# Kernel optimization log

Measured on AMD Instinct MI355X. Metric: run time of the kernel, lower is better.

## Reference

```python
import jax, jax.numpy as jnp
import numpy as np

B, EMBED, HEADS, T = 2, 512, 8, 2048
DH = EMBED // HEADS
EPS = 1e-5
# NOTE: torch code computes embed_dim // num_heads ** 0.5 == 512 // sqrt(8)
SCALE = EMBED // HEADS ** 0.5  # = 181.0, reproduced faithfully


def ws_conv1x1(x, w, b, mask):
    # weight-standardized 1x1 conv; w: [O, I], x: [B, I, T], mask: [B, T]
    mu = jnp.mean(w, axis=1, keepdims=True)
    var = jnp.var(w, axis=1, keepdims=True)
    wn = (w - mu) * jax.lax.rsqrt(var + EPS)
    x = x * mask[:, None, :].astype(x.dtype)
    return jnp.einsum('oi,bit->bot', wn, x) + b[None, :, None]


def ln_head(x, g, b):
    # per-head LayerNorm over head dim; x: [B, H, DH, T], normalized over DH
    xt = jnp.swapaxes(x, -1, -2)  # [B, H, T, DH]
    mu = jnp.mean(xt, axis=-1, keepdims=True)
    var = jnp.var(xt, axis=-1, keepdims=True)
    xn = (xt - mu) * jax.lax.rsqrt(var + EPS) * g + b
    return jnp.swapaxes(xn, -1, -2)


def setup_inputs():
    key = jax.random.key(0)
    ks = jax.random.split(key, 12)
    sc = 1.0 / np.sqrt(EMBED)
    d = {
        'q': jax.random.normal(ks[0], (B, EMBED, T), jnp.float32),
        'k': jax.random.normal(ks[1], (B, EMBED, T), jnp.float32),
        'v': jax.random.normal(ks[2], (B, EMBED, T), jnp.float32),
        'query_mask': jax.random.randint(ks[3], (B, T), 0, 2, jnp.int32),
        'key_mask': jax.random.randint(ks[4], (B, T), 0, 2, jnp.int32),
        'value_mask': jax.random.randint(ks[5], (B, T), 0, 2, jnp.int32),
        'Wq': jax.random.normal(ks[6], (EMBED, EMBED), jnp.float32) * sc,
        'bq': jnp.zeros((EMBED,), jnp.float32),
        'Wk': jax.random.normal(ks[7], (EMBED, EMBED), jnp.float32) * sc,
        'bk': jnp.zeros((EMBED,), jnp.float32),
        'Wv': jax.random.normal(ks[8], (EMBED, EMBED), jnp.float32) * sc,
        'bv': jnp.zeros((EMBED,), jnp.float32),
        'Wo': jax.random.normal(ks[9], (EMBED, EMBED), jnp.float32) * sc,
        'bo': jnp.zeros((EMBED,), jnp.float32),
        'ln_gq': jnp.ones((DH,), jnp.float32), 'ln_bq': jnp.zeros((DH,), jnp.float32),
        'ln_gk': jnp.ones((DH,), jnp.float32), 'ln_bk': jnp.zeros((DH,), jnp.float32),
        'ln_gv': jnp.ones((DH,), jnp.float32), 'ln_bv': jnp.zeros((DH,), jnp.float32),
    }
    return d


def reference(q, k, v, query_mask, key_mask, value_mask,
              Wq, bq, Wk, bk, Wv, bv, Wo, bo,
              ln_gq, ln_bq, ln_gk, ln_bk, ln_gv, ln_bv):
    q = ws_conv1x1(q, Wq, bq, query_mask)   # [B, E, T]
    k = ws_conv1x1(k, Wk, bk, key_mask)
    v = ws_conv1x1(v, Wv, bv, value_mask)
    # split heads: [B, E, T] -> [B, H, DH, T]
    q = q.reshape(B, HEADS, DH, T)
    k = k.reshape(B, HEADS, DH, T)
    v = v.reshape(B, HEADS, DH, T)
    # middle_norm: per-head LayerNorm over DH
    q = ln_head(q, ln_gq, ln_bq)
    k = ln_head(k, ln_gk, ln_bk)
    v = ln_head(v, ln_gv, ln_bv)
    # scores = q^T k / scale : [B, H, Tq, Tk]
    scores = jnp.einsum('bhdq,bhdk->bhqk', q, k) / SCALE
    scores = jnp.where(key_mask[:, None, None, :] == 0, -1e9, scores)
    scores = jax.nn.softmax(scores, axis=-1)
    scores = jnp.where(query_mask[:, None, :, None] == 0, 0.0, scores)
    # out = (scores @ v^T)^T : [B, H, DH, Tq]
    out = jnp.einsum('bhqk,bhdk->bhdq', scores, v)
    out = out.reshape(B, EMBED, T)
    out = ws_conv1x1(out, Wo, bo, query_mask)
    return out
```

## Files before the change

### kernel.cpp

```cpp
#include <hip/hip_runtime.h>


typedef __bf16 bf16;
typedef __bf16 bf16x8 __attribute__((ext_vector_type(8)));
typedef _Float16 f16;
typedef _Float16 f16x4 __attribute__((ext_vector_type(4)));
typedef float  f32x4  __attribute__((ext_vector_type(4)));

#define MFMA_BF16(a, b, c) __builtin_amdgcn_mfma_f32_16x16x32_bf16((a), (b), (c), 0, 0, 0)
#define MFMA_F16_K16(a, b, c) __builtin_amdgcn_mfma_f32_16x16x16f16((a), (b), (c), 0, 0, 0)

#define NB   2
#define NE   512
#define NH   8
#define NT   2048
#define NDH  64

__device__ __forceinline__ void gl_lds16(const bf16* g, bf16* l) {
  __builtin_amdgcn_global_load_lds(
      (const __attribute__((address_space(1))) void*)g,
      (__attribute__((address_space(3))) void*)l, 16, 0, 0);
}

__global__ __launch_bounds__(64) void k_wstd(
    const float* __restrict__ Wq, const float* __restrict__ Wk,
    const float* __restrict__ Wv, const float* __restrict__ Wo,
    const int* __restrict__ km,
    bf16* __restrict__ out, float* __restrict__ kmf)
{
  if (blockIdx.y == 4) {
    int idx = blockIdx.x * 64 + threadIdx.x;
    if (idx < NB * NT) kmf[idx] = (float)km[idx];
    return;
  }
  const float* W = blockIdx.y == 0 ? Wq : blockIdx.y == 1 ? Wk
                 : blockIdx.y == 2 ? Wv : Wo;
  int row = blockIdx.x, lane = threadIdx.x;
  const float4* p = (const float4*)(W + row * NE) + lane * 2;
  float4 a = p[0], c = p[1];
  float s  = a.x + a.y + a.z + a.w + c.x + c.y + c.z + c.w;
  float ss = a.x*a.x + a.y*a.y + a.z*a.z + a.w*a.w
           + c.x*c.x + c.y*c.y + c.z*c.z + c.w*c.w;
#pragma unroll
  for (int m = 1; m < 64; m <<= 1) { s += __shfl_xor(s, m); ss += __shfl_xor(ss, m); }
  float mean = s * (1.0f / NE);
  float var  = ss * (1.0f / NE) - mean * mean;
  float rstd = rsqrtf(var + 1e-5f);
  bf16x8 o;
  o[0] = (bf16)((a.x - mean) * rstd); o[1] = (bf16)((a.y - mean) * rstd);
  o[2] = (bf16)((a.z - mean) * rstd); o[3] = (bf16)((a.w - mean) * rstd);
  o[4] = (bf16)((c.x - mean) * rstd); o[5] = (bf16)((c.y - mean) * rstd);
  o[6] = (bf16)((c.z - mean) * rstd); o[7] = (bf16)((c.w - mean) * rstd);
  *(bf16x8*)(out + blockIdx.y * (NE * NE) + row * NE + lane * 8) = o;
}

__global__ __launch_bounds__(256) void k_trans(
    const float* __restrict__ q, const float* __restrict__ k,
    const float* __restrict__ v,
    const int* __restrict__ qm, const int* __restrict__ km,
    const int* __restrict__ vm,
    bf16* __restrict__ xT)
{
  int src = blockIdx.z >> 1, b = blockIdx.z & 1;
  const float* x = src == 0 ? q : src == 1 ? k : v;
  const int*   m = src == 0 ? qm : src == 1 ? km : vm;
  x += (size_t)b * NE * NT;
  m += b * NT;
  int t0 = blockIdx.x * 64, i0 = blockIdx.y * 64;
  __shared__ float tile[64][65];
  int tt = threadIdx.x & 63, ii = threadIdx.x >> 6;
#pragma unroll
  for (int i = ii; i < 64; i += 4)
    tile[i][tt] = x[(size_t)(i0 + i) * NT + t0 + tt];
  __syncthreads();
  bf16* o = xT + ((size_t)src * NB + b) * NT * NE;
  int i2 = threadIdx.x & 63, t2 = threadIdx.x >> 6;
#pragma unroll
  for (int t = t2; t < 64; t += 4) {
    float mk = (float)m[t0 + t];
    o[(size_t)(t0 + t) * NE + i0 + i2] = (bf16)(tile[i2][t] * mk);
  }
}

__global__ __launch_bounds__(256) void k_proj(
    const bf16* __restrict__ Wn,
    const bf16* __restrict__ xT,
    const float* __restrict__ bq, const float* __restrict__ bk,
    const float* __restrict__ bv,
    const float* __restrict__ gq, const float* __restrict__ bbq,
    const float* __restrict__ gk, const float* __restrict__ bbk,
    const float* __restrict__ gv, const float* __restrict__ bbv,
    bf16* __restrict__ Qh, bf16* __restrict__ Kh, f16* __restrict__ Vh)
{
  int src = blockIdx.z >> 1, b = blockIdx.z & 1;
  const bf16* A  = Wn + src * (NE * NE);
  const bf16* Bm = xT + ((size_t)src * NB + b) * NT * NE;
  int m0 = blockIdx.y * 64, n0 = blockIdx.x * 128;
  int h = m0 >> 6;

  __shared__ __align__(16) char smem[64 * 130 * 4 + 2 * 128 * 4];
  bf16*  Al = (bf16*)smem;
  bf16*  Bl = (bf16*)(smem + 8192);
  float* Yl = (float*)smem;
  float* mu = (float*)(smem + 64 * 130 * 4);
  float* rs = mu + 128;

  int tid = threadIdx.x, lane = tid & 63, w = tid >> 6;
  int mh = (w & 1) * 32, nh = (w >> 1) * 64;
  f32x4 acc[2][4] = {};

  for (int k0 = 0; k0 < NE; k0 += 64) {
    __syncthreads();
#pragma unroll
    for (int i = 0; i < 2; i++) {
      int row = (w << 4) + (i << 3) + (lane >> 3);
      int chg = (lane & 7) ^ (row & 7);
      gl_lds16(A + (m0 + row) * NE + k0 + (chg << 3),
               Al + ((w << 4) + (i << 3)) * 64);
    }
#pragma unroll
    for (int i = 0; i < 4; i++) {
      int row = (w << 5) + (i << 3) + (lane >> 3);
      int chg = (lane & 7) ^ (row & 7);
      gl_lds16(Bm + (size_t)(n0 + row) * NE + k0 + (chg << 3),
               Bl + ((w << 5) + (i << 3)) * 64);
    }
    __syncthreads();
#pragma unroll
    for (int kk = 0; kk < 64; kk += 32) {
      bf16x8 af[2], bfv[4];
#pragma unroll
      for (int ms = 0; ms < 2; ms++) {
        int row = mh + ms * 16 + (lane & 15);
        af[ms] = *(const bf16x8*)(Al + row * 64 +
                   ((((kk >> 3) + (lane >> 4)) ^ (row & 7)) << 3));
      }
#pragma unroll
      for (int ns = 0; ns < 4; ns++) {
        int row = nh + ns * 16 + (lane & 15);
        bfv[ns] = *(const bf16x8*)(Bl + row * 64 +
                   ((((kk >> 3) + (lane >> 4)) ^ (row & 7)) << 3));
      }
#pragma unroll
      for (int ms = 0; ms < 2; ms++)
#pragma unroll
        for (int ns = 0; ns < 4; ns++)
          acc[ms][ns] = MFMA_BF16(af[ms], bfv[ns], acc[ms][ns]);
    }
  }

  __syncthreads();
  {
    const float* bias = src == 0 ? bq : src == 1 ? bk : bv;
#pragma unroll
    for (int ms = 0; ms < 2; ms++)
#pragma unroll
      for (int ns = 0; ns < 4; ns++)
#pragma unroll
        for (int r = 0; r < 4; r++) {
          int om = mh + ms * 16 + ((lane >> 4) << 2) + r;
          int on = nh + ns * 16 + (lane & 15);
          Yl[om * 130 + on] = acc[ms][ns][r] + bias[m0 + om];
        }
  }
  __syncthreads();
  if (tid < 128) {
    float s = 0.f, ss = 0.f;
#pragma unroll 8
    for (int o = 0; o < 64; o++) { float y = Yl[o * 130 + tid]; s += y; ss += y * y; }
    float mean = s * (1.0f / 64.0f);
    float var  = ss * (1.0f / 64.0f) - mean * mean;
    mu[tid] = mean;
    rs[tid] = rsqrtf(var + 1e-5f);
  }
  __syncthreads();

  if (src < 2) {
    float scl = (src == 0) ? (1.0f / 181.0f) : 1.0f;
    const float* g  = src == 0 ? gq  : gk;
    const float* bb = src == 0 ? bbq : bbk;
    bf16* out = (src == 0 ? Qh : Kh) + ((size_t)(b * NH + h) * NT + n0) * NDH;
    int d = tid & 63, tb = tid >> 6;
    float gg = g[d] * scl, bb2 = bb[d] * scl;
#pragma unroll
    for (int t = tb; t < 128; t += 4) {
      float val = (Yl[d * 130 + t] - mu[t]) * rs[t] * gg + bb2;
      out[(size_t)t * NDH + d] = (bf16)val;
    }
  } else {
    f16* out = Vh + (size_t)(b * NH + h) * NDH * NT + n0;
    int t = tid & 127, db = tid >> 7;
#pragma unroll
    for (int d = db; d < 64; d += 2) {
      float val = (Yl[d * 130 + t] - mu[t]) * rs[t] * gv[d] + bbv[d];
      out[(size_t)d * NT + t] = (f16)val;
    }
  }
}

__global__ __launch_bounds__(256, 2) void k_attn(
    const bf16* __restrict__ Qh, const bf16* __restrict__ Kh,
    const f16* __restrict__ Vh,
    const float* __restrict__ kmf, const int* __restrict__ qmask,
    bf16* __restrict__ xa)
{
  int bh = blockIdx.y, b = bh >> 3, h = bh & 7;
  int q0 = blockIdx.x * 64;
  const bf16* Q = Qh + (size_t)bh * NT * NDH;
  const bf16* K = Kh + (size_t)bh * NT * NDH;
  const f16*  V = Vh + (size_t)bh * NDH * NT;

  __shared__ __align__(16) char smem[2 * 64 * 68 * 4 + 4 * 64 * 4];
  float* OlA  = (float*)smem;
  float* OlB  = (float*)(smem + 64 * 68 * 4);
  float* denl = (float*)(smem + 2 * 64 * 68 * 4);

  int tid = threadIdx.x, lane = tid & 63, w = tid >> 6;
  int quad = lane >> 4, l15 = lane & 15;
  const int ko = w * 32;

  bf16x8 qb[4][2];
#pragma unroll
  for (int qs = 0; qs < 4; qs++)
#pragma unroll
    for (int hf = 0; hf < 2; hf++)
      qb[qs][hf] = *(const bf16x8*)(Q + (size_t)(q0 + qs * 16 + l15) * NDH + hf * 32 + quad * 8);

  const bf16*  Kb = K + (size_t)(ko + l15) * NDH + quad * 8;
  const f16*   Vb = V + (size_t)l15 * NT + ko + quad * 4;
  const float* Mb = kmf + b * NT + ko + quad * 4;

  f32x4 acco[4][4] = {};
  float den[4] = {};

  bf16x8 ka[2][2];
  f16x4  vb[4][2];
#pragma unroll
  for (int kt = 0; kt < 2; kt++)
#pragma unroll
    for (int hf = 0; hf < 2; hf++)
      ka[kt][hf] = *(const bf16x8*)(Kb + (size_t)(kt * 16) * NDH + hf * 32);
#pragma unroll
  for (int ds = 0; ds < 4; ds++)
#pragma unroll
    for (int kt = 0; kt < 2; kt++)
      vb[ds][kt] = *(const f16x4*)(Vb + (size_t)(ds * 16) * NT + kt * 16);

  for (int k0 = 0; k0 < NT; k0 += 128) {
    int k1 = (k0 + 128) & (NT - 1);
    bf16x8 nka[2][2];
    f16x4  nvb[4][2];
#pragma unroll
    for (int kt = 0; kt < 2; kt++)
#pragma unroll
      for (int hf = 0; hf < 2; hf++)
        nka[kt][hf] = *(const bf16x8*)(Kb + (size_t)(k1 + kt * 16) * NDH + hf * 32);
#pragma unroll
    for (int ds = 0; ds < 4; ds++)
#pragma unroll
      for (int kt = 0; kt < 2; kt++)
        nvb[ds][kt] = *(const f16x4*)(Vb + (size_t)(ds * 16) * NT + k1 + kt * 16);

    float4 kmv0 = *(const float4*)(Mb + k0);
    float4 kmv1 = *(const float4*)(Mb + k0 + 16);

#pragma unroll
    for (int kt = 0; kt < 2; kt++) {
      const float4 kmv = kt ? kmv1 : kmv0;
      f32x4 s[4];
#pragma unroll
      for (int qs = 0; qs < 4; qs++) {
        f32x4 z = {};
        z = MFMA_BF16(ka[kt][0], qb[qs][0], z);
        z = MFMA_BF16(ka[kt][1], qb[qs][1], z);
        s[qs] = z;
      }
      f16x4 pa[4];
#pragma unroll
      for (int qs = 0; qs < 4; qs++) {
        float p0 = __expf(s[qs][0]) * kmv.x;
        float p1 = __expf(s[qs][1]) * kmv.y;
        float p2 = __expf(s[qs][2]) * kmv.z;
        float p3 = __expf(s[qs][3]) * kmv.w;
        den[qs] += (p0 + p1) + (p2 + p3);
        f16x4 pv; pv[0] = (f16)p0; pv[1] = (f16)p1; pv[2] = (f16)p2; pv[3] = (f16)p3;
        pa[qs] = pv;
      }
#pragma unroll
      for (int qs = 0; qs < 4; qs++)
#pragma unroll
        for (int ds = 0; ds < 4; ds++)
          acco[qs][ds] = MFMA_F16_K16(pa[qs], vb[ds][kt], acco[qs][ds]);
    }

#pragma unroll
    for (int kt = 0; kt < 2; kt++)
#pragma unroll
      for (int hf = 0; hf < 2; hf++)
        ka[kt][hf] = nka[kt][hf];
#pragma unroll
    for (int ds = 0; ds < 4; ds++)
#pragma unroll
      for (int kt = 0; kt < 2; kt++)
        vb[ds][kt] = nvb[ds][kt];
  }

#pragma unroll
  for (int qs = 0; qs < 4; qs++) {
    den[qs] += __shfl_xor(den[qs], 16);
    den[qs] += __shfl_xor(den[qs], 32);
  }
  if (quad == 0)
#pragma unroll
    for (int qs = 0; qs < 4; qs++)
      denl[w * 64 + qs * 16 + l15] = den[qs];

  float* Obuf = (w < 2) ? OlA : OlB;
  if ((w & 1) == 0) {
#pragma unroll
    for (int qs = 0; qs < 4; qs++)
#pragma unroll
      for (int ds = 0; ds < 4; ds++)
#pragma unroll
        for (int r = 0; r < 4; r++)
          Obuf[(qs * 16 + quad * 4 + r) * 68 + ds * 16 + l15] = acco[qs][ds][r];
  }
  __syncthreads();
  if (w & 1) {
#pragma unroll
    for (int qs = 0; qs < 4; qs++)
#pragma unroll
      for (int ds = 0; ds < 4; ds++)
#pragma unroll
        for (int r = 0; r < 4; r++)
          Obuf[(qs * 16 + quad * 4 + r) * 68 + ds * 16 + l15] += acco[qs][ds][r];
  }
  __syncthreads();

#pragma unroll
  for (int i = 0; i < 16; i++) {
    int ql = w * 16 + i;
    float dtot = denl[ql] + denl[64 + ql] + denl[128 + ql] + denl[192 + ql];
    float qm = (float)qmask[b * NT + q0 + ql];
    float inv = qm / dtot;
    float val = (OlA[ql * 68 + lane] + OlB[ql * 68 + lane]) * inv;
    xa[((size_t)b * NT + q0 + ql) * NE + h * NDH + lane] = (bf16)val;
  }
}

__global__ __launch_bounds__(256) void k_oproj(
    const bf16* __restrict__ A,
    const bf16* __restrict__ xab,
    const float* __restrict__ bo, float* __restrict__ out)
{
  int b = blockIdx.z;
  const bf16* Bm = xab + (size_t)b * NT * NE;
  int m0 = blockIdx.y * 64, n0 = blockIdx.x * 64;

  __shared__ __align__(16) char smem[16384];
  bf16* Al = (bf16*)smem;
  bf16* Bl = (bf16*)(smem + 8192);

  int tid = threadIdx.x, lane = tid & 63, w = tid >> 6;
  int mh = (w & 1) * 32, nh = (w >> 1) * 32;
  f32x4 acc[2][2] = {};

  for (int k0 = 0; k0 < NE; k0 += 64) {
    __syncthreads();
#pragma unroll
    for (int i = 0; i < 2; i++) {
      int row = (w << 4) + (i << 3) + (lane >> 3);
      int chg = (lane & 7) ^ (row & 7);
      gl_lds16(A + (m0 + row) * NE + k0 + (chg << 3),
               Al + ((w << 4) + (i << 3)) * 64);
    }
#pragma unroll
    for (int i = 0; i < 2; i++) {
      int row = (w << 4) + (i << 3) + (lane >> 3);
      int chg = (lane & 7) ^ (row & 7);
      gl_lds16(Bm + (size_t)(n0 + row) * NE + k0 + (chg << 3),
               Bl + ((w << 4) + (i << 3)) * 64);
    }
    __syncthreads();
#pragma unroll
    for (int kk = 0; kk < 64; kk += 32) {
      bf16x8 af[2], bfv[2];
#pragma unroll
      for (int ms = 0; ms < 2; ms++) {
        int row = mh + ms * 16 + (lane & 15);
        af[ms] = *(const bf16x8*)(Al + row * 64 +
                   ((((kk >> 3) + (lane >> 4)) ^ (row & 7)) << 3));
      }
#pragma unroll
      for (int ns = 0; ns < 2; ns++) {
        int row = nh + ns * 16 + (lane & 15);
        bfv[ns] = *(const bf16x8*)(Bl + row * 64 +
                   ((((kk >> 3) + (lane >> 4)) ^ (row & 7)) << 3));
      }
#pragma unroll
      for (int ms = 0; ms < 2; ms++)
#pragma unroll
        for (int ns = 0; ns < 2; ns++)
          acc[ms][ns] = MFMA_BF16(af[ms], bfv[ns], acc[ms][ns]);
    }
  }

#pragma unroll
  for (int ms = 0; ms < 2; ms++)
#pragma unroll
    for (int ns = 0; ns < 2; ns++)
#pragma unroll
      for (int r = 0; r < 4; r++) {
        int o = m0 + mh + ms * 16 + ((lane >> 4) << 2) + r;
        int t = n0 + nh + ns * 16 + (lane & 15);
        out[(size_t)b * NE * NT + (size_t)o * NT + t] = acc[ms][ns][r] + bo[o];
      }
}

extern "C" void kernel_launch(void* const* d_in, const int* in_sizes, int n_in,
                              void* d_out, int out_size, void* d_ws, size_t ws_size,
                              hipStream_t stream)
{
  const float* q  = (const float*)d_in[0];
  const float* k  = (const float*)d_in[1];
  const float* v  = (const float*)d_in[2];
  const int*   qm = (const int*)d_in[3];
  const int*   km = (const int*)d_in[4];
  const int*   vm = (const int*)d_in[5];
  const float* Wq = (const float*)d_in[6];  const float* bq = (const float*)d_in[7];
  const float* Wk = (const float*)d_in[8];  const float* bk = (const float*)d_in[9];
  const float* Wv = (const float*)d_in[10]; const float* bv = (const float*)d_in[11];
  const float* Wo = (const float*)d_in[12]; const float* bo = (const float*)d_in[13];
  const float* gq = (const float*)d_in[14]; const float* bbq = (const float*)d_in[15];
  const float* gk = (const float*)d_in[16]; const float* bbk = (const float*)d_in[17];
  const float* gv = (const float*)d_in[18]; const float* bbv = (const float*)d_in[19];
  float* out = (float*)d_out;

  char* wsb = (char*)d_ws;
  bf16*  Wn  = (bf16*)(wsb);
  bf16*  xT  = (bf16*)(wsb + (2ull  << 20));
  bf16*  Qh  = (bf16*)(wsb + (14ull << 20));
  bf16*  Kh  = (bf16*)(wsb + (18ull << 20));
  f16*   Vh  = (f16*) (wsb + (22ull << 20));
  bf16*  xa  = (bf16*)(wsb + (26ull << 20));
  float* kmf = (float*)(wsb + (30ull << 20));

  k_wstd <<<dim3(512, 5),   64,  0, stream>>>(Wq, Wk, Wv, Wo, km, Wn, kmf);
  k_trans<<<dim3(32, 8, 6), 256, 0, stream>>>(q, k, v, qm, km, vm, xT);
  k_proj <<<dim3(16, 8, 6), 256, 0, stream>>>(Wn, xT, bq, bk, bv,
                                              gq, bbq, gk, bbk, gv, bbv,
                                              Qh, Kh, Vh);
  k_attn <<<dim3(32, 16),   256, 0, stream>>>(Qh, Kh, Vh, kmf, qm, xa);
  k_oproj<<<dim3(32, 8, 2), 256, 0, stream>>>(Wn + 3 * NE * NE, xa, bo, out);
}
```

Baseline: 187.8 us.

## Halve attention query tile, use exp2 with folded log2e, vectorize transpose

The attention kernel now processes 32 queries per block instead of 64 and launches twice as many blocks with a higher occupancy hint. The goal is better CU fill on a grid that was only 512 blocks, at the cost of reloading K and V twice as often per query. The softmax exponent now uses a native exp2, with log2(e) folded into the Q scale in the projection kernel. The input transpose kernel reads with float4 loads and writes bf16 pairs, reducing the number of memory instructions.

```diff
diff --git a/kernel.cpp b/kernel.cpp
--- a/kernel.cpp
+++ b/kernel.cpp
@@ -2,6 +2,7 @@
 
 
 typedef __bf16 bf16;
+typedef __bf16 bf16x2 __attribute__((ext_vector_type(2)));
 typedef __bf16 bf16x8 __attribute__((ext_vector_type(8)));
 typedef _Float16 f16;
 typedef _Float16 f16x4 __attribute__((ext_vector_type(4)));
@@ -9,6 +10,12 @@
 
 #define MFMA_BF16(a, b, c) __builtin_amdgcn_mfma_f32_16x16x32_bf16((a), (b), (c), 0, 0, 0)
 #define MFMA_F16_K16(a, b, c) __builtin_amdgcn_mfma_f32_16x16x16f16((a), (b), (c), 0, 0, 0)
+
+#if __has_builtin(__builtin_amdgcn_exp2f)
+#define EXP2F(x) __builtin_amdgcn_exp2f(x)
+#else
+#define EXP2F(x) __expf((x) * 0.6931471805599453f)
+#endif
 
 #define NB   2
 #define NE   512
@@ -68,17 +75,25 @@
   m += b * NT;
   int t0 = blockIdx.x * 64, i0 = blockIdx.y * 64;
   __shared__ float tile[64][65];
-  int tt = threadIdx.x & 63, ii = threadIdx.x >> 6;
-#pragma unroll
-  for (int i = ii; i < 64; i += 4)
-    tile[i][tt] = x[(size_t)(i0 + i) * NT + t0 + tt];
+  int lr = threadIdx.x >> 4;
+  int tc = (threadIdx.x & 15) * 4;
+#pragma unroll
+  for (int p = 0; p < 4; p++) {
+    int row = p * 16 + lr;
+    float4 v4 = *(const float4*)(x + (size_t)(i0 + row) * NT + t0 + tc);
+    tile[row][tc]     = v4.x; tile[row][tc + 1] = v4.y;
+    tile[row][tc + 2] = v4.z; tile[row][tc + 3] = v4.w;
+  }
   __syncthreads();
   bf16* o = xT + ((size_t)src * NB + b) * NT * NE;
-  int i2 = threadIdx.x & 63, t2 = threadIdx.x >> 6;
-#pragma unroll
-  for (int t = t2; t < 64; t += 4) {
+  int i2 = (threadIdx.x & 31) * 2, t2 = threadIdx.x >> 5;
+#pragma unroll
+  for (int t = t2; t < 64; t += 8) {
     float mk = (float)m[t0 + t];
-    o[(size_t)(t0 + t) * NE + i0 + i2] = (bf16)(tile[i2][t] * mk);
+    bf16x2 w2;
+    w2[0] = (bf16)(tile[i2][t] * mk);
+    w2[1] = (bf16)(tile[i2 + 1][t] * mk);
+    *(bf16x2*)(o + (size_t)(t0 + t) * NE + i0 + i2) = w2;
   }
 }
 
@@ -176,7 +191,7 @@
   __syncthreads();
 
   if (src < 2) {
-    float scl = (src == 0) ? (1.0f / 181.0f) : 1.0f;
+    float scl = (src == 0) ? (1.4426950408889634f / 181.0f) : 1.0f;
     const float* g  = src == 0 ? gq  : gk;
     const float* bb = src == 0 ? bbq : bbk;
     bf16* out = (src == 0 ? Qh : Kh) + ((size_t)(b * NH + h) * NT + n0) * NDH;
@@ -198,30 +213,30 @@
   }
 }
 
-__global__ __launch_bounds__(256, 2) void k_attn(
+__global__ __launch_bounds__(256, 4) void k_attn(
     const bf16* __restrict__ Qh, const bf16* __restrict__ Kh,
     const f16* __restrict__ Vh,
     const float* __restrict__ kmf, const int* __restrict__ qmask,
     bf16* __restrict__ xa)
 {
   int bh = blockIdx.y, b = bh >> 3, h = bh & 7;
-  int q0 = blockIdx.x * 64;
+  int q0 = blockIdx.x * 32;
   const bf16* Q = Qh + (size_t)bh * NT * NDH;
   const bf16* K = Kh + (size_t)bh * NT * NDH;
   const f16*  V = Vh + (size_t)bh * NDH * NT;
 
-  __shared__ __align__(16) char smem[2 * 64 * 68 * 4 + 4 * 64 * 4];
+  __shared__ __align__(16) char smem[2 * 32 * 68 * 4 + 4 * 32 * 4];
   float* OlA  = (float*)smem;
-  float* OlB  = (float*)(smem + 64 * 68 * 4);
-  float* denl = (float*)(smem + 2 * 64 * 68 * 4);
+  float* OlB  = (float*)(smem + 32 * 68 * 4);
+  float* denl = (float*)(smem + 2 * 32 * 68 * 4);
 
   int tid = threadIdx.x, lane = tid & 63, w = tid >> 6;
   int quad = lane >> 4, l15 = lane & 15;
   const int ko = w * 32;
 
-  bf16x8 qb[4][2];
-#pragma unroll
-  for (int qs = 0; qs < 4; qs++)
+  bf16x8 qb[2][2];
+#pragma unroll
+  for (int qs = 0; qs < 2; qs++)
 #pragma unroll
     for (int hf = 0; hf < 2; hf++)
       qb[qs][hf] = *(const bf16x8*)(Q + (size_t)(q0 + qs * 16 + l15) * NDH + hf * 32 + quad * 8);
@@ -230,8 +245,8 @@
   const f16*   Vb = V + (size_t)l15 * NT + ko + quad * 4;
   const float* Mb = kmf + b * NT + ko + quad * 4;
 
-  f32x4 acco[4][4] = {};
-  float den[4] = {};
+  f32x4 acco[2][4] = {};
+  float den[2] = {};
 
   bf16x8 ka[2][2];
   f16x4  vb[4][2];
@@ -267,27 +282,27 @@
 #pragma unroll
     for (int kt = 0; kt < 2; kt++) {
       const float4 kmv = kt ? kmv1 : kmv0;
-      f32x4 s[4];
-#pragma unroll
-      for (int qs = 0; qs < 4; qs++) {
+      f32x4 s[2];
+#pragma unroll
+      for (int qs = 0; qs < 2; qs++) {
         f32x4 z = {};
         z = MFMA_BF16(ka[kt][0], qb[qs][0], z);
         z = MFMA_BF16(ka[kt][1], qb[qs][1], z);
         s[qs] = z;
       }
-      f16x4 pa[4];
-#pragma unroll
-      for (int qs = 0; qs < 4; qs++) {
-        float p0 = __expf(s[qs][0]) * kmv.x;
-        float p1 = __expf(s[qs][1]) * kmv.y;
-        float p2 = __expf(s[qs][2]) * kmv.z;
-        float p3 = __expf(s[qs][3]) * kmv.w;
+      f16x4 pa[2];
+#pragma unroll
+      for (int qs = 0; qs < 2; qs++) {
+        float p0 = EXP2F(s[qs][0]) * kmv.x;
+        float p1 = EXP2F(s[qs][1]) * kmv.y;
+        float p2 = EXP2F(s[qs][2]) * kmv.z;
+        float p3 = EXP2F(s[qs][3]) * kmv.w;
         den[qs] += (p0 + p1) + (p2 + p3);
         f16x4 pv; pv[0] = (f16)p0; pv[1] = (f16)p1; pv[2] = (f16)p2; pv[3] = (f16)p3;
         pa[qs] = pv;
       }
 #pragma unroll
-      for (int qs = 0; qs < 4; qs++)
+      for (int qs = 0; qs < 2; qs++)
 #pragma unroll
         for (int ds = 0; ds < 4; ds++)
           acco[qs][ds] = MFMA_F16_K16(pa[qs], vb[ds][kt], acco[qs][ds]);
@@ -306,19 +321,19 @@
   }
 
 #pragma unroll
-  for (int qs = 0; qs < 4; qs++) {
+  for (int qs = 0; qs < 2; qs++) {
     den[qs] += __shfl_xor(den[qs], 16);
     den[qs] += __shfl_xor(den[qs], 32);
   }
   if (quad == 0)
 #pragma unroll
-    for (int qs = 0; qs < 4; qs++)
-      denl[w * 64 + qs * 16 + l15] = den[qs];
+    for (int qs = 0; qs < 2; qs++)
+      denl[w * 32 + qs * 16 + l15] = den[qs];
 
   float* Obuf = (w < 2) ? OlA : OlB;
   if ((w & 1) == 0) {
 #pragma unroll
-    for (int qs = 0; qs < 4; qs++)
+    for (int qs = 0; qs < 2; qs++)
 #pragma unroll
       for (int ds = 0; ds < 4; ds++)
 #pragma unroll
@@ -328,7 +343,7 @@
   __syncthreads();
   if (w & 1) {
 #pragma unroll
-    for (int qs = 0; qs < 4; qs++)
+    for (int qs = 0; qs < 2; qs++)
 #pragma unroll
       for (int ds = 0; ds < 4; ds++)
 #pragma unroll
@@ -338,9 +353,9 @@
   __syncthreads();
 
 #pragma unroll
-  for (int i = 0; i < 16; i++) {
-    int ql = w * 16 + i;
-    float dtot = denl[ql] + denl[64 + ql] + denl[128 + ql] + denl[192 + ql];
+  for (int i = 0; i < 8; i++) {
+    int ql = w * 8 + i;
+    float dtot = denl[ql] + denl[32 + ql] + denl[64 + ql] + denl[96 + ql];
     float qm = (float)qmask[b * NT + q0 + ql];
     float inv = qm / dtot;
     float val = (OlA[ql * 68 + lane] + OlB[ql * 68 + lane]) * inv;
@@ -450,6 +465,6 @@
   k_proj <<<dim3(16, 8, 6), 256, 0, stream>>>(Wn, xT, bq, bk, bv,
                                               gq, bbq, gk, bbk, gv, bbv,
                                               Qh, Kh, Vh);
-  k_attn <<<dim3(32, 16),   256, 0, stream>>>(Qh, Kh, Vh, kmf, qm, xa);
+  k_attn <<<dim3(64, 16),   256, 0, stream>>>(Qh, Kh, Vh, kmf, qm, xa);
   k_oproj<<<dim3(32, 8, 2), 256, 0, stream>>>(Wn + 3 * NE * NE, xa, bo, out);
 }
```

New measurement: 223.6 us. +19.1%, slower.
